# Optimization experiments

Measured on AMD Instinct MI355X. Metric: run time of the kernel, lower is better.

The kernel has to match this reference:

```python
import jax, jax.numpy as jnp
import numpy as np

E = 16           # num_experts
D = 4096         # hidden_size
F = 688          # per-expert SwiGLU intermediate size
N = 8192         # total tokens (bsz*seq_len)
CAP_FACTOR = 1.25


def setup_inputs() -> dict:
    key = jax.random.key(0)
    k1, k2, k3, k4, k5, k6 = jax.random.split(key, 6)
    return {
        "x": jax.random.normal(k1, (N, D), dtype=jnp.float32),
        "topk_idx": jax.random.randint(k2, (N,), 0, E, dtype=jnp.int32),
        "topk_scores": jax.random.uniform(k3, (N,), dtype=jnp.float32),
        "Wg": jax.random.normal(k4, (E, D, F), dtype=jnp.float32) * 0.02,
        "Wu": jax.random.normal(k5, (E, D, F), dtype=jnp.float32) * 0.02,
        "Wd": jax.random.normal(k6, (E, F, D), dtype=jnp.float32) * 0.02,
    }


def reference(x, topk_idx, topk_scores, Wg, Wu, Wd):
    # Switch-style top-1 MoE with capacity-based token dropping.
    # Deterministic variant: tokens beyond capacity are dropped in token order
    # (original uses randperm; the math pattern is identical).
    n, d = x.shape
    e = Wg.shape[0]
    cap = int(CAP_FACTOR * n / e)  # static under jit

    # position of each token within its assigned expert (0-based)
    oh = jax.nn.one_hot(topk_idx, e, dtype=jnp.int32)            # [N, E]
    pos = jnp.take_along_axis(jnp.cumsum(oh, axis=0) - 1,
                              topk_idx[:, None].astype(jnp.int32), axis=1)[:, 0]
    keep = pos < cap                                             # [N] bool

    # dispatch: scatter kept tokens into [E, cap, D]; dropped go to dummy row E
    e_safe = jnp.where(keep, topk_idx, e)
    p_safe = jnp.minimum(pos, cap - 1)
    buf = jnp.zeros((e + 1, cap, d), x.dtype).at[e_safe, p_safe].set(x)[:e]

    # per-expert SwiGLU FFN: down(silu(gate(x)) * up(x))
    h = jax.nn.silu(jnp.einsum('ecd,edf->ecf', buf, Wg)) \
        * jnp.einsum('ecd,edf->ecf', buf, Wu)                    # [E, cap, F]
    out = jnp.einsum('ecf,efd->ecd', h, Wd)                      # [E, cap, D]

    # combine: gather back, zero-pad dropped tokens, scale by gate scores
    y = out[topk_idx, p_safe] * keep[:, None].astype(x.dtype)
    y = y * topk_scores[:, None]
    return y
```

## Files before the change

kernel.cpp:

```cpp
#include <hip/hip_runtime.h>
#include <hip/hip_bf16.h>

#define E_ 16
#define D_ 4096
#define F_ 688
#define N_ 8192
#define CAP_ 640
#define NFT_ 11
#define NKT32_ 128
#define NFT32_ 22

typedef __attribute__((ext_vector_type(8))) short bf16x8;
typedef __attribute__((ext_vector_type(4))) float f32x4;
typedef __attribute__((ext_vector_type(4))) float fvec4;
typedef __attribute__((ext_vector_type(4))) unsigned short usvec4;
typedef __attribute__((ext_vector_type(8))) unsigned short usvec8;

__device__ __forceinline__ unsigned short f2bf(float f) {
    __hip_bfloat16 h = __float2bfloat16(f);
    return __builtin_bit_cast(unsigned short, h);
}
__device__ __forceinline__ void gload16(const unsigned short* g, unsigned short* l) {
    __builtin_amdgcn_global_load_lds(
        (const __attribute__((address_space(1))) unsigned int*)g,
        (__attribute__((address_space(3))) unsigned int*)l, 16, 0, 0);
}

#define WAITVN(N) asm volatile("s_waitcnt vmcnt(" #N ")" ::: "memory")
#define SBAR      __builtin_amdgcn_s_barrier()
#define SCHED0    __builtin_amdgcn_sched_barrier(0)


__global__ void k_dispatch(const int* __restrict__ idx,
                           int* __restrict__ slot_token,
                           int* __restrict__ row_of,
                           int* __restrict__ cnt) {
    __shared__ int hist[256][E_];
    const int t = threadIdx.x;
#pragma unroll
    for (int e = 0; e < E_; e++) hist[t][e] = 0;
    __syncthreads();
    const int base = t * (N_ / 256);
    for (int j = 0; j < N_ / 256; j++) {
        int e = idx[base + j];
        hist[t][e]++;
    }
    __syncthreads();
    if (t < E_) {
        int run = 0;
        for (int i = 0; i < 256; i++) { int v = hist[i][t]; hist[i][t] = run; run += v; }
        cnt[t] = run < CAP_ ? run : CAP_;
    }
    for (int s = t; s < E_ * CAP_; s += 256) slot_token[s] = -1;
    __syncthreads();
    for (int j = 0; j < N_ / 256; j++) {
        int i = base + j;
        int e = idx[i];
        int p = hist[t][e]++;
        if (p < CAP_) { slot_token[e * CAP_ + p] = i; row_of[i] = e * CAP_ + p; }
        else          { row_of[i] = -1; }
    }
}

__global__ void k_zero_dropped(const int* __restrict__ row_of, float* __restrict__ y) {
    for (int i = blockIdx.x; i < N_; i += gridDim.x) {
        if (row_of[i] >= 0) continue;
        fvec4* yp = (fvec4*)(y + (size_t)i * D_);
        fvec4 z = {0.f, 0.f, 0.f, 0.f};
        for (int c = threadIdx.x; c < D_ / 4; c += 256) yp[c] = z;
    }
}

__global__ void k_gather(const float* __restrict__ x, const int* __restrict__ slot_token,
                         unsigned short* __restrict__ Aimg) {
    const int strip = blockIdx.y;
    const int kg = blockIdx.x;
    const int t = threadIdx.x;
    const int r = t >> 1, h = t & 1;
    const int tok = slot_token[strip * 128 + r];
#pragma unroll
    for (int i = 0; i < 8; i++) {
        const int kt = kg * 8 + i;
        unsigned short* dst = Aimg + ((size_t)strip * NKT32_ + kt) * 4096;
        usvec8 p0, p1;
        if (tok < 0) {
            usvec8 z = {0, 0, 0, 0, 0, 0, 0, 0};
            p0 = z; p1 = z;
        } else {
            const float* src = x + (size_t)tok * D_ + kt * 32 + h * 16;
            fvec4 a = *(const fvec4*)(src);
            fvec4 b = *(const fvec4*)(src + 4);
            fvec4 c = *(const fvec4*)(src + 8);
            fvec4 d = *(const fvec4*)(src + 12);
            usvec8 q0 = {f2bf(a[0]), f2bf(a[1]), f2bf(a[2]), f2bf(a[3]),
                         f2bf(b[0]), f2bf(b[1]), f2bf(b[2]), f2bf(b[3])};
            usvec8 q1 = {f2bf(c[0]), f2bf(c[1]), f2bf(c[2]), f2bf(c[3]),
                         f2bf(d[0]), f2bf(d[1]), f2bf(d[2]), f2bf(d[3])};
            p0 = q0; p1 = q1;
        }
        *(usvec8*)&dst[(2 * h) * 1024 + r * 8]     = p0;
        *(usvec8*)&dst[(2 * h + 1) * 1024 + r * 8] = p1;
    }
}

__global__ void k_wprep_gu(const float* __restrict__ Wg, const float* __restrict__ Wu,
                           unsigned short* __restrict__ img) {
    const int ft = blockIdx.x, kt = blockIdx.y, e = blockIdx.z;
    const int tid = threadIdx.x;
    const int f4 = (tid & 15) * 4, kq4 = (tid >> 4) * 4;
    const int gf = ft * 64 + f4;
    const bool v = gf < F_;
    const fvec4 fz = {0.f, 0.f, 0.f, 0.f};
    fvec4 g[4], u[4];
#pragma unroll
    for (int r = 0; r < 4; r++) {
        size_t off = (size_t)e * D_ * F_ + (size_t)(kt * 64 + kq4 + r) * F_ + gf;
        g[r] = v ? *(const fvec4*)(Wg + off) : fz;
        u[r] = v ? *(const fvec4*)(Wu + off) : fz;
    }
    const int t32 = kq4 >> 5, kl = kq4 & 31;
    unsigned short* dst = img + ((size_t)(e * NKT32_ + kt * 2 + t32) * NFT_ + ft) * 4096;
    const int ubase = (kl >> 3) * 512 + (kl & 7);
#pragma unroll
    for (int i = 0; i < 4; i++) {
        usvec4 pg = {f2bf(g[0][i]), f2bf(g[1][i]), f2bf(g[2][i]), f2bf(g[3][i])};
        usvec4 pu = {f2bf(u[0][i]), f2bf(u[1][i]), f2bf(u[2][i]), f2bf(u[3][i])};
        *(usvec4*)&dst[ubase + (f4 + i) * 8]        = pg;
        *(usvec4*)&dst[2048 + ubase + (f4 + i) * 8] = pu;
    }
}

__global__ void k_wprep_d(const float* __restrict__ Wd, unsigned short* __restrict__ img) {
    const int dt = blockIdx.x, kt = blockIdx.y, e = blockIdx.z;
    const int tid = threadIdx.x;
    const int d4 = (tid & 15) * 4, kq4 = (tid >> 4) * 4;
    const int gd = dt * 64 + d4;
    const fvec4 fz = {0.f, 0.f, 0.f, 0.f};
    fvec4 b[4];
#pragma unroll
    for (int r = 0; r < 4; r++) {
        int krow = kt * 64 + kq4 + r;
        b[r] = (krow < F_) ? *(const fvec4*)(Wd + (size_t)e * F_ * D_ + (size_t)krow * D_ + gd) : fz;
    }
    const int t32 = kq4 >> 5, kl = kq4 & 31;
    unsigned short* dst = img + ((size_t)(e * NFT32_ + kt * 2 + t32) * 64 + dt) * 2048;
    const int ubase = (kl >> 3) * 512 + (kl & 7);
#pragma unroll
    for (int i = 0; i < 4; i++) {
        usvec4 p = {f2bf(b[0][i]), f2bf(b[1][i]), f2bf(b[2][i]), f2bf(b[3][i])};
        *(usvec4*)&dst[ubase + (d4 + i) * 8] = p;
    }
}

__global__ __launch_bounds__(256, 3) void k_gemm1_dma(
    const unsigned short* __restrict__ Aimg, const unsigned short* __restrict__ Wgu,
    const int* __restrict__ cnt, unsigned short* __restrict__ Himg) {
    const int bid = blockIdx.x;
    const int xcd = bid & 7;
    const int j = bid >> 3;
    const int mb = j % 5;
    const int gl = j / 5;
    const int group = xcd * 22 + gl;
    const int e = group / NFT_, fidx = group % NFT_;
    const int m0 = mb * 128;
    if (m0 >= cnt[e]) return;
    const int strip = e * 5 + mb;

    __shared__ __align__(16) unsigned short Bgu[3][8192];

    const int tid = threadIdx.x;
    const int lane = tid & 63, wave = tid >> 6;
    const int wm = wave >> 1, wn = wave & 1;
    const int wq = wave * 1024;

    f32x4 accG[4][2], accU[4][2];
#pragma unroll
    for (int a = 0; a < 4; a++)
#pragma unroll
        for (int b = 0; b < 2; b++) {
            f32x4 z = {0.f, 0.f, 0.f, 0.f};
            accG[a][b] = z; accU[a][b] = z;
        }

    const unsigned short* Astrip = Aimg + (size_t)strip * NKT32_ * 4096;
    const unsigned short* WguE = Wgu + ((size_t)e * NKT32_ * NFT_ + fidx) * 4096;
    const int GUS = NFT_ * 4096;
    const int afo = (lane >> 4) * 1024 + (wm * 64 + (lane & 15)) * 8;
    const int bfo = (lane >> 4) * 512 + (wn * 32 + (lane & 15)) * 8;

    bf16x8 a0[8], a1[8];

#define LOADA1(T, S)                                                             \
    {                                                                            \
        const unsigned short* ab = Astrip + (size_t)(2 * (T)) * 4096 + afo;      \
        _Pragma("unroll") for (int mi = 0; mi < 4; mi++) {                       \
            S[mi]     = *(const bf16x8*)(ab + mi * 128);                         \
            S[mi + 4] = *(const bf16x8*)(ab + 4096 + mi * 128);                  \
        }                                                                        \
    }
#define DMAB1(T, BUF)                                                            \
    {                                                                            \
        const unsigned short* b0 = WguE + (size_t)(2 * (T)) * GUS + wq;          \
        gload16(b0 + lane * 8,       &Bgu[BUF][wq]);                             \
        gload16(b0 + 512 + lane * 8, &Bgu[BUF][wq + 512]);                       \
        const unsigned short* b1 = b0 + GUS;                                     \
        gload16(b1 + lane * 8,       &Bgu[BUF][4096 + wq]);                      \
        gload16(b1 + 512 + lane * 8, &Bgu[BUF][4096 + wq + 512]);                \
    }
#define MFMAS1(BUF, S)                                                           \
    {                                                                            \
        __builtin_amdgcn_s_setprio(1);                                           \
        _Pragma("unroll") for (int kh = 0; kh < 2; kh++) {                       \
            bf16x8 bg[2], bu[2];                                                 \
            _Pragma("unroll") for (int ni = 0; ni < 2; ni++) {                   \
                bg[ni] = *(const bf16x8*)&Bgu[BUF][kh * 4096 + bfo + ni * 128];  \
                bu[ni] = *(const bf16x8*)&Bgu[BUF][kh * 4096 + 2048 + bfo + ni * 128]; \
            }                                                                    \
            _Pragma("unroll") for (int mi = 0; mi < 4; mi++)                     \
            _Pragma("unroll") for (int ni = 0; ni < 2; ni++) {                   \
                accG[mi][ni] = __builtin_amdgcn_mfma_f32_16x16x32_bf16(S[kh * 4 + mi], bg[ni], accG[mi][ni], 0, 0, 0); \
                accU[mi][ni] = __builtin_amdgcn_mfma_f32_16x16x32_bf16(S[kh * 4 + mi], bu[ni], accU[mi][ni], 0, 0, 0); \
            }                                                                    \
        }                                                                        \
        __builtin_amdgcn_s_setprio(0);                                           \
    }
#define G1IT(T, CS, NS, WN)                                                      \
    {                                                                            \
        SBAR;                                                                    \
        if ((T) + 1 < 64) { LOADA1((T) + 1, NS) }                                \
        if ((T) + 2 < 64) { const int nb_ = ((T) + 2) % 3; DMAB1((T) + 2, nb_) } \
        SCHED0;                                                                  \
        WAITVN(WN);                                                              \
        SCHED0;                                                                  \
        { const int cb_ = (T) % 3; MFMAS1(cb_, CS) }                             \
    }

    LOADA1(0, a0)
    SCHED0;
    DMAB1(0, 0)
    DMAB1(1, 1)
    SCHED0;

    for (int m = 0; m < 31; m++) {
        G1IT(2 * m,     a0, a1, 16)
        G1IT(2 * m + 1, a1, a0, 16)
    }
    G1IT(62, a0, a1, 12)
    G1IT(63, a1, a0, 0)
#undef G1IT
#undef MFMAS1
#undef DMAB1
#undef LOADA1

    unsigned short* Hs = Himg + (size_t)(strip * NFT32_ + fidx * 2) * 4096;
#pragma unroll
    for (int mi = 0; mi < 4; mi++)
#pragma unroll
        for (int ni = 0; ni < 2; ni++) {
            int fl = wn * 32 + ni * 16 + (lane & 15);
            int rl = wm * 64 + mi * 16 + ((lane >> 4) << 2);
            unsigned short* Ht = Hs + (size_t)(fl >> 5) * 4096 + ((fl & 31) >> 3) * 1024 + (fl & 7);
#pragma unroll
            for (int q = 0; q < 4; q++) {
                float g = accG[mi][ni][q], u = accU[mi][ni][q];
                float h = g * u / (1.f + __expf(-g));
                Ht[(rl + q) * 8] = f2bf(h);
            }
        }
}

__global__ __launch_bounds__(256, 3) void k_gemm2_dma(
    const unsigned short* __restrict__ Himg, const unsigned short* __restrict__ WdI,
    const int* __restrict__ slot_token, const int* __restrict__ cnt,
    const float* __restrict__ scores, float* __restrict__ y) {
    const int bid = blockIdx.x;
    const int xcd = bid & 7;
    const int j = bid >> 3;
    const int mb = j % 5;
    const int gl = j / 5;
    const int group = xcd * 128 + gl;
    const int e = group >> 6, didx = group & 63;
    const int m0 = mb * 128, d0 = didx * 64;
    if (m0 >= cnt[e]) return;
    const int strip = e * 5 + mb;

    __shared__ __align__(16) unsigned short Bd[3][4096];
    __shared__ int tokS[128];
    __shared__ float scS[128];

    const int tid = threadIdx.x;
    const int lane = tid & 63, wave = tid >> 6;
    const int wm = wave >> 1, wn = wave & 1;

    if (tid < 128) {
        int t = slot_token[e * CAP_ + m0 + tid];
        tokS[tid] = t;
        scS[tid] = (t >= 0) ? scores[t] : 0.f;
    }
    __syncthreads();

    f32x4 acc[4][2];
#pragma unroll
    for (int a = 0; a < 4; a++)
#pragma unroll
        for (int b = 0; b < 2; b++) {
            f32x4 z = {0.f, 0.f, 0.f, 0.f};
            acc[a][b] = z;
        }

    const unsigned short* Hstrip = Himg + (size_t)strip * NFT32_ * 4096;
    const unsigned short* WdE = WdI + ((size_t)e * NFT32_ * 64 + didx) * 2048;
    const int WDS = 64 * 2048;
    const int afo = (lane >> 4) * 1024 + (wm * 64 + (lane & 15)) * 8;
    const int bfo = (lane >> 4) * 512 + (wn * 32 + (lane & 15)) * 8;

    bf16x8 a0[8], a1[8];

#define LOADA2(T, S)                                                             \
    {                                                                            \
        const unsigned short* ab = Hstrip + (size_t)(2 * (T)) * 4096 + afo;      \
        _Pragma("unroll") for (int mi = 0; mi < 4; mi++) {                       \
            S[mi]     = *(const bf16x8*)(ab + mi * 128);                         \
            S[mi + 4] = *(const bf16x8*)(ab + 4096 + mi * 128);                  \
        }                                                                        \
    }
#define DMAB2(T, BUF)                                                            \
    {                                                                            \
        const unsigned short* b0 = WdE + (size_t)(2 * (T)) * WDS + wave * 512;   \
        gload16(b0 + lane * 8,       &Bd[BUF][wave * 512]);                      \
        gload16(b0 + WDS + lane * 8, &Bd[BUF][2048 + wave * 512]);               \
    }
#define MFMAS2(BUF, S)                                                           \
    {                                                                            \
        __builtin_amdgcn_s_setprio(1);                                           \
        _Pragma("unroll") for (int kh = 0; kh < 2; kh++) {                       \
            bf16x8 bv[2];                                                        \
            _Pragma("unroll") for (int ni = 0; ni < 2; ni++)                     \
                bv[ni] = *(const bf16x8*)&Bd[BUF][kh * 2048 + bfo + ni * 128];   \
            _Pragma("unroll") for (int mi = 0; mi < 4; mi++)                     \
            _Pragma("unroll") for (int ni = 0; ni < 2; ni++)                     \
                acc[mi][ni] = __builtin_amdgcn_mfma_f32_16x16x32_bf16(S[kh * 4 + mi], bv[ni], acc[mi][ni], 0, 0, 0); \
        }                                                                        \
        __builtin_amdgcn_s_setprio(0);                                           \
    }
#define G2IT(T, CS, NS, WN)                                                      \
    {                                                                            \
        SBAR;                                                                    \
        if ((T) + 1 < 11) { LOADA2((T) + 1, NS) }                                \
        if ((T) + 2 < 11) { const int nb_ = ((T) + 2) % 3; DMAB2((T) + 2, nb_) } \
        SCHED0;                                                                  \
        WAITVN(WN);                                                              \
        SCHED0;                                                                  \
        { const int cb_ = (T) % 3; MFMAS2(cb_, CS) }                             \
    }

    LOADA2(0, a0)
    SCHED0;
    DMAB2(0, 0)
    DMAB2(1, 1)
    SCHED0;

    G2IT(0, a0, a1, 12)
    G2IT(1, a1, a0, 12)
    G2IT(2, a0, a1, 12)
    G2IT(3, a1, a0, 12)
    G2IT(4, a0, a1, 12)
    G2IT(5, a1, a0, 12)
    G2IT(6, a0, a1, 12)
    G2IT(7, a1, a0, 12)
    G2IT(8, a0, a1, 12)
    G2IT(9, a1, a0, 10)
    G2IT(10, a0, a1, 0)
#undef G2IT
#undef MFMAS2
#undef DMAB2
#undef LOADA2

#pragma unroll
    for (int mi = 0; mi < 4; mi++)
#pragma unroll
        for (int ni = 0; ni < 2; ni++) {
            int d = d0 + wn * 32 + ni * 16 + (lane & 15);
            int rowb = wm * 64 + mi * 16 + ((lane >> 4) << 2);
#pragma unroll
            for (int q = 0; q < 4; q++) {
                int row = rowb + q;
                int t = tokS[row];
                if (t >= 0) y[(size_t)t * D_ + d] = acc[mi][ni][q] * scS[row];
            }
        }
}

extern "C" void kernel_launch(void* const* d_in, const int* in_sizes, int n_in,
                              void* d_out, int out_size, void* d_ws, size_t ws_size,
                              hipStream_t stream) {
    const float* x   = (const float*)d_in[0];
    const int*   idx = (const int*)d_in[1];
    const float* sc  = (const float*)d_in[2];
    const float* Wg  = (const float*)d_in[3];
    const float* Wu  = (const float*)d_in[4];
    const float* Wd  = (const float*)d_in[5];
    float* y = (float*)d_out;

    char* ws = (char*)d_ws;
    int* slot_token = (int*)ws;
    int* row_of     = (int*)(ws + 40960);
    int* cnt        = (int*)(ws + 40960 + 32768);
    const size_t hoff   = 131072;
    const size_t hbytes = (size_t)80 * NFT32_ * 8192;
    unsigned short* Himg = (unsigned short*)(ws + hoff);
    const size_t aoff   = hoff + hbytes;
    const size_t abytes = (size_t)80 * NKT32_ * 8192;
    unsigned short* Aimg = (unsigned short*)(ws + aoff);
    const size_t guoff   = aoff + abytes;
    const size_t gubytes = (size_t)E_ * NKT32_ * NFT_ * 8192;
    unsigned short* WguI = (unsigned short*)(ws + guoff);
    const size_t wdoff   = guoff + gubytes;
    unsigned short* WdI  = (unsigned short*)(ws + wdoff);

    k_dispatch<<<1, 256, 0, stream>>>(idx, slot_token, row_of, cnt);
    k_zero_dropped<<<128, 256, 0, stream>>>(row_of, y);
    k_gather<<<dim3(16, 80), 256, 0, stream>>>(x, slot_token, Aimg);
    k_wprep_gu<<<dim3(NFT_, 64, E_), 256, 0, stream>>>(Wg, Wu, WguI);
    k_wprep_d<<<dim3(64, NFT_, E_), 256, 0, stream>>>(Wd, WdI);
    k_gemm1_dma<<<880, 256, 0, stream>>>(Aimg, WguI, cnt, Himg);
    k_gemm2_dma<<<5120, 256, 0, stream>>>(Himg, WdI, slot_token, cnt, sc, y);
}
```

Before: 518.5 us.

## Split K across waves in both MoE GEMMs with LDS reduction of accumulators

Both GEMM kernels change the wave decomposition from a 2x2 M/N split to an M split crossed with a K-half split. Each wave now covers the full N tile for its K half and loads a quarter of the A fragments. Partial accumulators are then combined through an LDS reduction that reuses the B staging buffer. The wait/barrier ordering in the pipeline moves the vmcnt wait before the barrier. Because the accumulator arrays double, gemm1 launch bounds drop to 2 blocks per CU, which risks lower occupancy and adds reduction barriers in exchange for fewer global A loads per MFMA.

```diff
diff --git a/kernel.cpp b/kernel.cpp
--- a/kernel.cpp
+++ b/kernel.cpp
@@ -152,7 +152,7 @@
     }
 }
 
-__global__ __launch_bounds__(256, 3) void k_gemm1_dma(
+__global__ __launch_bounds__(256, 2) void k_gemm1_dma(
     const unsigned short* __restrict__ Aimg, const unsigned short* __restrict__ Wgu,
     const int* __restrict__ cnt, unsigned short* __restrict__ Himg) {
     const int bid = blockIdx.x;
@@ -170,14 +170,13 @@
 
     const int tid = threadIdx.x;
     const int lane = tid & 63, wave = tid >> 6;
-    const int wm = wave >> 1, wn = wave & 1;
-    const int wq = wave * 1024;
-
-    f32x4 accG[4][2], accU[4][2];
+    const int wm = wave & 1, kh = wave >> 1;
+
+    f32x4 accG[4][4], accU[4][4];
 #pragma unroll
     for (int a = 0; a < 4; a++)
 #pragma unroll
-        for (int b = 0; b < 2; b++) {
+        for (int b = 0; b < 4; b++) {
             f32x4 z = {0.f, 0.f, 0.f, 0.f};
             accG[a][b] = z; accU[a][b] = z;
         }
@@ -186,53 +185,49 @@
     const unsigned short* WguE = Wgu + ((size_t)e * NKT32_ * NFT_ + fidx) * 4096;
     const int GUS = NFT_ * 4096;
     const int afo = (lane >> 4) * 1024 + (wm * 64 + (lane & 15)) * 8;
-    const int bfo = (lane >> 4) * 512 + (wn * 32 + (lane & 15)) * 8;
-
-    bf16x8 a0[8], a1[8];
+    const int bfo = (lane >> 4) * 512 + (lane & 15) * 8;
+
+    bf16x8 a0[4], a1[4];
 
 #define LOADA1(T, S)                                                             \
     {                                                                            \
-        const unsigned short* ab = Astrip + (size_t)(2 * (T)) * 4096 + afo;      \
-        _Pragma("unroll") for (int mi = 0; mi < 4; mi++) {                       \
-            S[mi]     = *(const bf16x8*)(ab + mi * 128);                         \
-            S[mi + 4] = *(const bf16x8*)(ab + 4096 + mi * 128);                  \
+        const unsigned short* ab = Astrip + (size_t)(2 * (T) + kh) * 4096 + afo; \
+        _Pragma("unroll") for (int mf = 0; mf < 4; mf++)                         \
+            S[mf] = *(const bf16x8*)(ab + mf * 128);                             \
+    }
+#define DMAB1(T, BUF)                                                            \
+    {                                                                            \
+        const unsigned short* bA = WguE + (size_t)(2 * (T)) * GUS;               \
+        const unsigned short* bB = bA + GUS;                                     \
+        _Pragma("unroll") for (int i = 0; i < 4; i++) {                          \
+            const int c = wave * 4 + i;                                          \
+            const unsigned short* src = (c < 8) ? (bA + c * 512) : (bB + (c - 8) * 512); \
+            gload16(src + lane * 8, &Bgu[BUF][c * 512]);                         \
         }                                                                        \
     }
-#define DMAB1(T, BUF)                                                            \
-    {                                                                            \
-        const unsigned short* b0 = WguE + (size_t)(2 * (T)) * GUS + wq;          \
-        gload16(b0 + lane * 8,       &Bgu[BUF][wq]);                             \
-        gload16(b0 + 512 + lane * 8, &Bgu[BUF][wq + 512]);                       \
-        const unsigned short* b1 = b0 + GUS;                                     \
-        gload16(b1 + lane * 8,       &Bgu[BUF][4096 + wq]);                      \
-        gload16(b1 + 512 + lane * 8, &Bgu[BUF][4096 + wq + 512]);                \
-    }
 #define MFMAS1(BUF, S)                                                           \
     {                                                                            \
         __builtin_amdgcn_s_setprio(1);                                           \
-        _Pragma("unroll") for (int kh = 0; kh < 2; kh++) {                       \
-            bf16x8 bg[2], bu[2];                                                 \
-            _Pragma("unroll") for (int ni = 0; ni < 2; ni++) {                   \
-                bg[ni] = *(const bf16x8*)&Bgu[BUF][kh * 4096 + bfo + ni * 128];  \
-                bu[ni] = *(const bf16x8*)&Bgu[BUF][kh * 4096 + 2048 + bfo + ni * 128]; \
-            }                                                                    \
-            _Pragma("unroll") for (int mi = 0; mi < 4; mi++)                     \
-            _Pragma("unroll") for (int ni = 0; ni < 2; ni++) {                   \
-                accG[mi][ni] = __builtin_amdgcn_mfma_f32_16x16x32_bf16(S[kh * 4 + mi], bg[ni], accG[mi][ni], 0, 0, 0); \
-                accU[mi][ni] = __builtin_amdgcn_mfma_f32_16x16x32_bf16(S[kh * 4 + mi], bu[ni], accU[mi][ni], 0, 0, 0); \
-            }                                                                    \
+        bf16x8 bg[4], bu[4];                                                     \
+        _Pragma("unroll") for (int nf = 0; nf < 4; nf++) {                       \
+            bg[nf] = *(const bf16x8*)&Bgu[BUF][kh * 4096 + bfo + nf * 128];      \
+            bu[nf] = *(const bf16x8*)&Bgu[BUF][kh * 4096 + 2048 + bfo + nf * 128]; \
+        }                                                                        \
+        _Pragma("unroll") for (int mf = 0; mf < 4; mf++)                         \
+        _Pragma("unroll") for (int nf = 0; nf < 4; nf++) {                       \
+            accG[mf][nf] = __builtin_amdgcn_mfma_f32_16x16x32_bf16(S[mf], bg[nf], accG[mf][nf], 0, 0, 0); \
+            accU[mf][nf] = __builtin_amdgcn_mfma_f32_16x16x32_bf16(S[mf], bu[nf], accU[mf][nf], 0, 0, 0); \
         }                                                                        \
         __builtin_amdgcn_s_setprio(0);                                           \
     }
-#define G1IT(T, CS, NS, WN)                                                      \
-    {                                                                            \
+#define G1IT(T, CS, NS, WN, HA, HB)                                              \
+    {                                                                            \
+        WAITVN(WN);                                                              \
         SBAR;                                                                    \
-        if ((T) + 1 < 64) { LOADA1((T) + 1, NS) }                                \
-        if ((T) + 2 < 64) { const int nb_ = ((T) + 2) % 3; DMAB1((T) + 2, nb_) } \
+        if (HA) { LOADA1((T) + 1, NS) }                                          \
+        if (HB) { DMAB1((T) + 2, ((T) + 2) % 3) }                                \
         SCHED0;                                                                  \
-        WAITVN(WN);                                                              \
-        SCHED0;                                                                  \
-        { const int cb_ = (T) % 3; MFMAS1(cb_, CS) }                             \
+        MFMAS1((T) % 3, CS)                                                      \
     }
 
     LOADA1(0, a0)
@@ -242,27 +237,62 @@
     SCHED0;
 
     for (int m = 0; m < 31; m++) {
-        G1IT(2 * m,     a0, a1, 16)
-        G1IT(2 * m + 1, a1, a0, 16)
-    }
-    G1IT(62, a0, a1, 12)
-    G1IT(63, a1, a0, 0)
+        G1IT(2 * m,     a0, a1, 4, 1, 1)
+        G1IT(2 * m + 1, a1, a0, 4, 1, 1)
+    }
+    G1IT(62, a0, a1, 4, 1, 0)
+    G1IT(63, a1, a0, 0, 0, 0)
 #undef G1IT
 #undef MFMAS1
 #undef DMAB1
 #undef LOADA1
 
+    {
+        float* red = (float*)(&Bgu[0][0]);
+        __syncthreads();
+#pragma unroll
+        for (int mf = 0; mf < 4; mf++)
+#pragma unroll
+            for (int nfl = 0; nfl < 2; nfl++)
+                *(f32x4*)&red[(((wm * 2 + (1 - kh)) * 4 + mf) * 2 + nfl) * 256 + lane * 4] =
+                    accG[mf][2 * (1 - kh) + nfl];
+        __syncthreads();
+#pragma unroll
+        for (int mf = 0; mf < 4; mf++)
+#pragma unroll
+            for (int nfl = 0; nfl < 2; nfl++) {
+                f32x4 p = *(const f32x4*)&red[(((wm * 2 + kh) * 4 + mf) * 2 + nfl) * 256 + lane * 4];
+                accG[mf][2 * kh + nfl] += p;
+            }
+        __syncthreads();
+#pragma unroll
+        for (int mf = 0; mf < 4; mf++)
+#pragma unroll
+            for (int nfl = 0; nfl < 2; nfl++)
+                *(f32x4*)&red[(((wm * 2 + (1 - kh)) * 4 + mf) * 2 + nfl) * 256 + lane * 4] =
+                    accU[mf][2 * (1 - kh) + nfl];
+        __syncthreads();
+#pragma unroll
+        for (int mf = 0; mf < 4; mf++)
+#pragma unroll
+            for (int nfl = 0; nfl < 2; nfl++) {
+                f32x4 p = *(const f32x4*)&red[(((wm * 2 + kh) * 4 + mf) * 2 + nfl) * 256 + lane * 4];
+                accU[mf][2 * kh + nfl] += p;
+            }
+    }
+
     unsigned short* Hs = Himg + (size_t)(strip * NFT32_ + fidx * 2) * 4096;
 #pragma unroll
-    for (int mi = 0; mi < 4; mi++)
-#pragma unroll
-        for (int ni = 0; ni < 2; ni++) {
-            int fl = wn * 32 + ni * 16 + (lane & 15);
-            int rl = wm * 64 + mi * 16 + ((lane >> 4) << 2);
+    for (int mf = 0; mf < 4; mf++)
+#pragma unroll
+        for (int nfl = 0; nfl < 2; nfl++) {
+            const int nf = 2 * kh + nfl;
+            int fl = nf * 16 + (lane & 15);
+            int rl = wm * 64 + mf * 16 + ((lane >> 4) << 2);
             unsigned short* Ht = Hs + (size_t)(fl >> 5) * 4096 + ((fl & 31) >> 3) * 1024 + (fl & 7);
 #pragma unroll
             for (int q = 0; q < 4; q++) {
-                float g = accG[mi][ni][q], u = accU[mi][ni][q];
+                float g = accG[mf][nf][q], u = accU[mf][nf][q];
                 float h = g * u / (1.f + __expf(-g));
                 Ht[(rl + q) * 8] = f2bf(h);
             }
@@ -290,7 +320,7 @@
 
     const int tid = threadIdx.x;
     const int lane = tid & 63, wave = tid >> 6;
-    const int wm = wave >> 1, wn = wave & 1;
+    const int wm = wave & 1, kh = wave >> 1;
 
     if (tid < 128) {
         int t = slot_token[e * CAP_ + m0 + tid];
@@ -299,11 +329,11 @@
     }
     __syncthreads();
 
-    f32x4 acc[4][2];
+    f32x4 acc[4][4];
 #pragma unroll
     for (int a = 0; a < 4; a++)
 #pragma unroll
-        for (int b = 0; b < 2; b++) {
+        for (int b = 0; b < 4; b++) {
             f32x4 z = {0.f, 0.f, 0.f, 0.f};
             acc[a][b] = z;
         }
@@ -312,46 +342,45 @@
     const unsigned short* WdE = WdI + ((size_t)e * NFT32_ * 64 + didx) * 2048;
     const int WDS = 64 * 2048;
     const int afo = (lane >> 4) * 1024 + (wm * 64 + (lane & 15)) * 8;
-    const int bfo = (lane >> 4) * 512 + (wn * 32 + (lane & 15)) * 8;
-
-    bf16x8 a0[8], a1[8];
+    const int bfo = (lane >> 4) * 512 + (lane & 15) * 8;
+
+    bf16x8 a0[4], a1[4];
 
 #define LOADA2(T, S)                                                             \
     {                                                                            \
-        const unsigned short* ab = Hstrip + (size_t)(2 * (T)) * 4096 + afo;      \
-        _Pragma("unroll") for (int mi = 0; mi < 4; mi++) {                       \
-            S[mi]     = *(const bf16x8*)(ab + mi * 128);                         \
-            S[mi + 4] = *(const bf16x8*)(ab + 4096 + mi * 128);                  \
+        const unsigned short* ab = Hstrip + (size_t)(2 * (T) + kh) * 4096 + afo; \
+        _Pragma("unroll") for (int mf = 0; mf < 4; mf++)                         \
+            S[mf] = *(const bf16x8*)(ab + mf * 128);                             \
+    }
+#define DMAB2(T, BUF)                                                            \
+    {                                                                            \
+        const unsigned short* bA = WdE + (size_t)(2 * (T)) * WDS;                \
+        const unsigned short* bB = bA + WDS;                                     \
+        _Pragma("unroll") for (int i = 0; i < 2; i++) {                          \
+            const int c = wave * 2 + i;                                          \
+            const unsigned short* src = (c < 4) ? (bA + c * 512) : (bB + (c - 4) * 512); \
+            gload16(src + lane * 8, &Bd[BUF][c * 512]);                          \
         }                                                                        \
     }
-#define DMAB2(T, BUF)                                                            \
-    {                                                                            \
-        const unsigned short* b0 = WdE + (size_t)(2 * (T)) * WDS + wave * 512;   \
-        gload16(b0 + lane * 8,       &Bd[BUF][wave * 512]);                      \
-        gload16(b0 + WDS + lane * 8, &Bd[BUF][2048 + wave * 512]);               \
-    }
 #define MFMAS2(BUF, S)                                                           \
     {                                                                            \
         __builtin_amdgcn_s_setprio(1);                                           \
-        _Pragma("unroll") for (int kh = 0; kh < 2; kh++) {                       \
-            bf16x8 bv[2];                                                        \
-            _Pragma("unroll") for (int ni = 0; ni < 2; ni++)                     \
-                bv[ni] = *(const bf16x8*)&Bd[BUF][kh * 2048 + bfo + ni * 128];   \
-            _Pragma("unroll") for (int mi = 0; mi < 4; mi++)                     \
-            _Pragma("unroll") for (int ni = 0; ni < 2; ni++)                     \
-                acc[mi][ni] = __builtin_amdgcn_mfma_f32_16x16x32_bf16(S[kh * 4 + mi], bv[ni], acc[mi][ni], 0, 0, 0); \
-        }                                                                        \
+        bf16x8 bv[4];                                                            \
+        _Pragma("unroll") for (int nf = 0; nf < 4; nf++)                         \
+            bv[nf] = *(const bf16x8*)&Bd[BUF][kh * 2048 + bfo + nf * 128];       \
+        _Pragma("unroll") for (int mf = 0; mf < 4; mf++)                         \
+        _Pragma("unroll") for (int nf = 0; nf < 4; nf++)                         \
+            acc[mf][nf] = __builtin_amdgcn_mfma_f32_16x16x32_bf16(S[mf], bv[nf], acc[mf][nf], 0, 0, 0); \
         __builtin_amdgcn_s_setprio(0);                                           \
     }
-#define G2IT(T, CS, NS, WN)                                                      \
-    {                                                                            \
+#define G2IT(T, CS, NS, WN, HA, HB)                                              \
+    {                                                                            \
+        WAITVN(WN);                                                              \
         SBAR;                                                                    \
-        if ((T) + 1 < 11) { LOADA2((T) + 1, NS) }                                \
-        if ((T) + 2 < 11) { const int nb_ = ((T) + 2) % 3; DMAB2((T) + 2, nb_) } \
+        if (HA) { LOADA2((T) + 1, NS) }                                          \
+        if (HB) { DMAB2((T) + 2, ((T) + 2) % 3) }                                \
         SCHED0;                                                                  \
-        WAITVN(WN);                                                              \
-        SCHED0;                                                                  \
-        { const int cb_ = (T) % 3; MFMAS2(cb_, CS) }                             \
+        MFMAS2((T) % 3, CS)                                                      \
     }
 
     LOADA2(0, a0)
@@ -360,33 +389,56 @@
     DMAB2(1, 1)
     SCHED0;
 
-    G2IT(0, a0, a1, 12)
-    G2IT(1, a1, a0, 12)
-    G2IT(2, a0, a1, 12)
-    G2IT(3, a1, a0, 12)
-    G2IT(4, a0, a1, 12)
-    G2IT(5, a1, a0, 12)
-    G2IT(6, a0, a1, 12)
-    G2IT(7, a1, a0, 12)
-    G2IT(8, a0, a1, 12)
-    G2IT(9, a1, a0, 10)
-    G2IT(10, a0, a1, 0)
+    G2IT(0, a0, a1, 2, 1, 1)
+    G2IT(1, a1, a0, 2, 1, 1)
+    G2IT(2, a0, a1, 2, 1, 1)
+    G2IT(3, a1, a0, 2, 1, 1)
+    G2IT(4, a0, a1, 2, 1, 1)
+    G2IT(5, a1, a0, 2, 1, 1)
+    G2IT(6, a0, a1, 2, 1, 1)
+    G2IT(7, a1, a0, 2, 1, 1)
+    G2IT(8, a0, a1, 2, 1, 1)
+    G2IT(9, a1, a0, 2, 1, 0)
+    G2IT(10, a0, a1, 0, 0, 0)
 #undef G2IT
 #undef MFMAS2
 #undef DMAB2
 #undef LOADA2
 
-#pragma unroll
-    for (int mi = 0; mi < 4; mi++)
-#pragma unroll
-        for (int ni = 0; ni < 2; ni++) {
-            int d = d0 + wn * 32 + ni * 16 + (lane & 15);
-            int rowb = wm * 64 + mi * 16 + ((lane >> 4) << 2);
+    {
+        float* red = (float*)(&Bd[0][0]);
+#pragma unroll
+        for (int mh = 0; mh < 2; mh++) {
+            __syncthreads();
+#pragma unroll
+            for (int mfl = 0; mfl < 2; mfl++)
+#pragma unroll
+                for (int nfl = 0; nfl < 2; nfl++)
+                    *(f32x4*)&red[((((wm * 2 + (1 - kh)) * 2 + mfl) * 2 + nfl)) * 256 + lane * 4] =
+                        acc[mh * 2 + mfl][2 * (1 - kh) + nfl];
+            __syncthreads();
+#pragma unroll
+            for (int mfl = 0; mfl < 2; mfl++)
+#pragma unroll
+                for (int nfl = 0; nfl < 2; nfl++) {
+                    f32x4 p = *(const f32x4*)&red[((((wm * 2 + kh) * 2 + mfl) * 2 + nfl)) * 256 + lane * 4];
+                    acc[mh * 2 + mfl][2 * kh + nfl] += p;
+                }
+        }
+    }
+
+#pragma unroll
+    for (int mf = 0; mf < 4; mf++)
+#pragma unroll
+        for (int nfl = 0; nfl < 2; nfl++) {
+            const int nf = 2 * kh + nfl;
+            int d = d0 + nf * 16 + (lane & 15);
+            int rowb = wm * 64 + mf * 16 + ((lane >> 4) << 2);
 #pragma unroll
             for (int q = 0; q < 4; q++) {
                 int row = rowb + q;
                 int t = tokS[row];
-                if (t >= 0) y[(size_t)t * D_ + d] = acc[mi][ni][q] * scS[row];
+                if (t >= 0) y[(size_t)t * D_ + d] = acc[mf][nf][q] * scS[row];
             }
         }
 }
```

Result: slower. 1.107 ms (+113.5%).
